# Kernel tuning notes

Hardware: AMD Instinct MI355X
Metric: run time of the kernel (lower is better)

Reference implementation:

```python
import jax, jax.numpy as jnp
import numpy as np

H = 16          # n_heads
D_MODEL = 1024
DK = D_MODEL // H  # 64
N = 2048        # total tokens (module flattens batch*seq)
NEG = -1000000000.0


def setup_inputs() -> dict:
    key = jax.random.key(0)
    ks = jax.random.split(key, 12)
    s = 1.0 / np.sqrt(D_MODEL)
    inp = {
        "query": jax.random.normal(ks[0], (N, D_MODEL), jnp.float32),
        "key": jax.random.normal(ks[1], (N, D_MODEL), jnp.float32),
        "value": jax.random.normal(ks[2], (N, D_MODEL), jnp.float32),
        "mask": jax.random.randint(ks[3], (1, N), 0, 2, jnp.int32),
        "Wq": jax.random.normal(ks[4], (D_MODEL, D_MODEL), jnp.float32) * s,
        "bq": jax.random.normal(ks[5], (D_MODEL,), jnp.float32) * 0.01,
        "Wk": jax.random.normal(ks[6], (D_MODEL, D_MODEL), jnp.float32) * s,
        "bk": jax.random.normal(ks[7], (D_MODEL,), jnp.float32) * 0.01,
        "Wv": jax.random.normal(ks[8], (D_MODEL, D_MODEL), jnp.float32) * s,
        "bv": jax.random.normal(ks[9], (D_MODEL,), jnp.float32) * 0.01,
        "Wo": jax.random.normal(ks[10], (D_MODEL, D_MODEL), jnp.float32) * s,
        "bo": jax.random.normal(ks[11], (D_MODEL,), jnp.float32) * 0.01,
    }
    return inp


def reference(query, key, value, mask, Wq, bq, Wk, bk, Wv, bv, Wo, bo):
    # Linear projections (torch Linear: x @ W.T + b), then split heads: (N, d_model) -> (h, N, d_k)
    def split_heads(x):
        return x.reshape(-1, H, DK).transpose(1, 0, 2)

    q = split_heads(query @ Wq.T + bq)
    k = split_heads(key @ Wk.T + bk)
    v = split_heads(value @ Wv.T + bv)

    # scaled dot-product attention: scores (h, N, N)
    scores = jnp.einsum("hnd,hmd->hnm", q, k) / jnp.sqrt(jnp.asarray(DK, q.dtype))
    # mask: (1, N) --unsqueeze(1)--> (1, 1, N), broadcast over (h, N, N)
    scores = jnp.where(mask[None, :, :] == 0, jnp.asarray(NEG, scores.dtype), scores)
    p_attn = jax.nn.softmax(scores, axis=-1)  # dropout identity (eval mode)

    x = jnp.einsum("hnm,hmd->hnd", p_attn, v)  # (h, N, d_k)
    x = x.transpose(1, 0, 2).reshape(-1, H * DK)  # (N, d_model)
    out = x @ Wo.T + bo
    return (out, p_attn)
```

## Files before the change

kernel.cpp:

```cpp
#include <hip/hip_runtime.h>


#define NTOK 2048
#define DMODEL 1024
#define NHEAD 16
#define DKH 64

typedef __attribute__((ext_vector_type(8))) short bf16x8;
typedef __attribute__((ext_vector_type(4))) float f32x4;

__device__ __forceinline__ unsigned short f2bf(float x) {
  unsigned int u = __builtin_bit_cast(unsigned int, x);
  u += 0x7fffu + ((u >> 16) & 1u);
  return (unsigned short)(u >> 16);
}

struct GemmP {
  const void* A[3];
  const void* B[3];
  const float* bias[3];
  long long sA, sB, sC;
  int lda, ldb, ldc;
  int M, Nn, K;
  const int* mask;
  float scale;
  void* C;
};

template<int ROWS, bool F32>
__device__ __forceinline__ void stage_tile(char* lds, const char* gsrc, int ld, int k0, int tid) {
  if constexpr (F32) {
    const float* src = (const float*)gsrc;
#pragma unroll
    for (int c = 0; c < ROWS / 16; ++c) {
      int cid = c * 256 + tid;
      int row = cid >> 4;
      int ck = cid & 15;
      float4 v = *(const float4*)(src + (size_t)row * ld + k0 + ck * 4);
      ushort4 h;
      h.x = f2bf(v.x); h.y = f2bf(v.y); h.z = f2bf(v.z); h.w = f2bf(v.w);
      int off = row * 128 + ((ck * 8) ^ ((row & 7) << 4));
      *(ushort4*)(lds + off) = h;
    }
  } else {
    const unsigned short* src = (const unsigned short*)gsrc;
#pragma unroll
    for (int c = 0; c < ROWS / 32; ++c) {
      int cid = c * 256 + tid;
      int row = cid >> 3;
      int ck = cid & 7;
      uint4 v = *(const uint4*)(src + (size_t)row * ld + k0 + ck * 8);
      int off = row * 128 + ((ck * 16) ^ ((row & 7) << 4));
      *(uint4*)(lds + off) = v;
    }
  }
}

__device__ __forceinline__ void stage_v256(char* lds, const unsigned short* src, int ld, int tid) {
#pragma unroll
  for (int c = 0; c < 4; ++c) {
    int cid = c * 256 + tid;
    int row = cid >> 4;
    int ck = cid & 15;
    uint4 v = *(const uint4*)(src + (size_t)row * ld + ck * 8);
    int off = row * 256 + ((ck * 16) ^ ((row & 7) << 4));
    *(uint4*)(lds + off) = v;
  }
}

__device__ __forceinline__ bf16x8 ldsfrag(const char* lds, int r, int kb) {
  return *(const bf16x8*)(lds + r * 128 + (kb ^ ((r & 7) << 4)));
}
__device__ __forceinline__ bf16x8 ldsfrag256(const char* lds, int r, int kb) {
  return *(const bf16x8*)(lds + r * 256 + (kb ^ ((r & 7) << 4)));
}

template<int BM, int BN, bool AF32, bool BF32, bool OUTF32, bool MASKED>
__global__ __launch_bounds__(256) void gemm_bt(GemmP P) {
  constexpr int BK = 64;
  constexpr int WM = BM / 2, WN = BN / 2, FM = WM / 16, FN = WN / 16;
  __shared__ char ldsA[BM * 128];
  __shared__ char ldsB[BN * 128];
  const int tid = threadIdx.x;
  const int z = blockIdx.z;
  const bool sel3 = (gridDim.z == 3);
  const int zi = sel3 ? z : 0;
  const int ntn = P.Nn / BN;
  const int bm = (int)blockIdx.x / ntn;
  const int bn = (int)blockIdx.x % ntn;
  const int m0 = bm * BM, n0 = bn * BN;

  const long long zA = sel3 ? 0 : (long long)z * P.sA;
  const long long zB = sel3 ? 0 : (long long)z * P.sB;
  const char* Ab = (const char*)P.A[zi] + ((long long)m0 * P.lda + zA) * (AF32 ? 4 : 2);
  const char* Bb = (const char*)P.B[zi] + ((long long)n0 * P.ldb + zB) * (BF32 ? 4 : 2);

  f32x4 acc[FM][FN] = {};
  const int lane = tid & 63;
  const int wm = (tid >> 6) >> 1, wn = (tid >> 6) & 1;

  for (int k0 = 0; k0 < P.K; k0 += BK) {
    stage_tile<BM, AF32>(ldsA, Ab, P.lda, k0, tid);
    stage_tile<BN, BF32>(ldsB, Bb, P.ldb, k0, tid);
    __syncthreads();
#pragma unroll
    for (int kk = 0; kk < 2; ++kk) {
      const int kb = kk * 64 + ((lane >> 4) * 16);
      bf16x8 a[FM], b[FN];
#pragma unroll
      for (int i = 0; i < FM; ++i) a[i] = ldsfrag(ldsA, wm * WM + i * 16 + (lane & 15), kb);
#pragma unroll
      for (int j = 0; j < FN; ++j) b[j] = ldsfrag(ldsB, wn * WN + j * 16 + (lane & 15), kb);
#pragma unroll
      for (int i = 0; i < FM; ++i)
#pragma unroll
        for (int j = 0; j < FN; ++j)
          acc[i][j] = __builtin_amdgcn_mfma_f32_16x16x32_bf16(a[i], b[j], acc[i][j], 0, 0, 0);
    }
    __syncthreads();
  }

  char* Cb = (char*)P.C + ((long long)z * P.sC) * (OUTF32 ? 4 : 2);
  const int rbase = m0 + wm * WM + ((lane >> 4) << 2);
  const int cbase = n0 + wn * WN + (lane & 15);
#pragma unroll
  for (int j = 0; j < FN; ++j) {
    const int col = cbase + j * 16;
    const float badd = P.bias[zi] ? P.bias[zi][col] : 0.0f;
    const bool msk = MASKED ? (P.mask[col] == 0) : false;
#pragma unroll
    for (int i = 0; i < FM; ++i) {
#pragma unroll
      for (int rg = 0; rg < 4; ++rg) {
        const int row = rbase + i * 16 + rg;
        float v = acc[i][j][rg] * P.scale + badd;
        if (MASKED && msk) v = -1000000000.0f;
        if constexpr (OUTF32)
          ((float*)Cb)[(size_t)row * P.ldc + col] = v;
        else
          ((unsigned short*)Cb)[(size_t)row * P.ldc + col] = f2bf(v);
      }
    }
  }
}

__global__ __launch_bounds__(256) void transpose_v(const unsigned short* __restrict__ VP,
                                                   unsigned short* __restrict__ VT) {
  __shared__ unsigned short t[64][72];
  const int h = blockIdx.y;
  const int n0 = blockIdx.x * 64;
  const int tid = threadIdx.x;
  const int rr = tid >> 3;
  const int cc = (tid & 7) * 8;
#pragma unroll
  for (int ps = 0; ps < 2; ++ps) {
    const int r = ps * 32 + rr;
    const unsigned short* src = VP + (size_t)(n0 + r) * DMODEL + h * DKH + cc;
    ushort4 a = *(const ushort4*)src;
    ushort4 b = *(const ushort4*)(src + 4);
    t[cc + 0][r] = a.x; t[cc + 1][r] = a.y; t[cc + 2][r] = a.z; t[cc + 3][r] = a.w;
    t[cc + 4][r] = b.x; t[cc + 5][r] = b.y; t[cc + 6][r] = b.z; t[cc + 7][r] = b.w;
  }
  __syncthreads();
#pragma unroll
  for (int ps = 0; ps < 2; ++ps) {
    const int d = ps * 32 + rr;
    unsigned short* dst = VT + ((size_t)h * DKH + d) * NTOK + n0 + cc;
    ushort4 a, b;
    a.x = t[d][cc + 0]; a.y = t[d][cc + 1]; a.z = t[d][cc + 2]; a.w = t[d][cc + 3];
    b.x = t[d][cc + 4]; b.y = t[d][cc + 5]; b.z = t[d][cc + 6]; b.w = t[d][cc + 7];
    *(ushort4*)dst = a;
    *(ushort4*)(dst + 4) = b;
  }
}

__global__ __launch_bounds__(256) void attn_fused(const unsigned short* __restrict__ QP,
                                                  const unsigned short* __restrict__ KP,
                                                  const unsigned short* __restrict__ VT,
                                                  const int* __restrict__ mask,
                                                  float* __restrict__ p,
                                                  unsigned short* __restrict__ XB) {
  __shared__ char ldsQ[64 * 128];
  __shared__ char ldsK[128 * 128];
  __shared__ char ldsV[64 * 256];
  __shared__ char ldsP[64 * 256];
  const int tid = threadIdx.x;
  const int lane = tid & 63;
  const int w = tid >> 6;
  const int l15 = lane & 15, lhi = lane >> 4;
  const int h = blockIdx.y;
  const int q0 = blockIdx.x * 64;
  const int mrow = w * 16 + l15;

  stage_tile<64, false>(ldsQ, (const char*)(QP + (size_t)q0 * DMODEL + h * DKH), DMODEL, 0, tid);
  __syncthreads();
  bf16x8 qf[2];
  qf[0] = ldsfrag(ldsQ, mrow, lhi * 16);
  qf[1] = ldsfrag(ldsQ, mrow, 64 + lhi * 16);

  float rsum = 0.0f;
  for (int it = 0; it < 16; ++it) {
    const int j0 = it * 128;
    __syncthreads();
    stage_tile<128, false>(ldsK, (const char*)(KP + (size_t)j0 * DMODEL + h * DKH), DMODEL, 0, tid);
    __syncthreads();
    f32x4 sacc[8] = {};
#pragma unroll
    for (int kk = 0; kk < 2; ++kk) {
#pragma unroll
      for (int js = 0; js < 8; ++js) {
        bf16x8 kf = ldsfrag(ldsK, js * 16 + l15, kk * 64 + lhi * 16);
        sacc[js] = __builtin_amdgcn_mfma_f32_16x16x32_bf16(kf, qf[kk], sacc[js], 0, 0, 0);
      }
    }
#pragma unroll
    for (int js = 0; js < 8; ++js) {
      int4 mv = *(const int4*)(mask + j0 + js * 16 + lhi * 4);
      rsum += (mv.x ? __expf(sacc[js][0] * 0.125f) : 0.0f);
      rsum += (mv.y ? __expf(sacc[js][1] * 0.125f) : 0.0f);
      rsum += (mv.z ? __expf(sacc[js][2] * 0.125f) : 0.0f);
      rsum += (mv.w ? __expf(sacc[js][3] * 0.125f) : 0.0f);
    }
  }
  rsum += __shfl_xor(rsum, 16, 64);
  rsum += __shfl_xor(rsum, 32, 64);
  const float rinv = 1.0f / rsum;

  float* prow = p + ((size_t)h * NTOK + q0 + mrow) * NTOK;
  f32x4 xacc[4] = {};
  for (int it = 0; it < 16; ++it) {
    const int j0 = it * 128;
    __syncthreads();
    stage_tile<128, false>(ldsK, (const char*)(KP + (size_t)j0 * DMODEL + h * DKH), DMODEL, 0, tid);
    stage_v256(ldsV, VT + (size_t)h * DKH * NTOK + j0, NTOK, tid);
    __syncthreads();
    f32x4 sacc[8] = {};
#pragma unroll
    for (int kk = 0; kk < 2; ++kk) {
#pragma unroll
      for (int js = 0; js < 8; ++js) {
        bf16x8 kf = ldsfrag(ldsK, js * 16 + l15, kk * 64 + lhi * 16);
        sacc[js] = __builtin_amdgcn_mfma_f32_16x16x32_bf16(kf, qf[kk], sacc[js], 0, 0, 0);
      }
    }
#pragma unroll
    for (int js = 0; js < 8; ++js) {
      int4 mv = *(const int4*)(mask + j0 + js * 16 + lhi * 4);
      float4 e;
      e.x = mv.x ? __expf(sacc[js][0] * 0.125f) * rinv : 0.0f;
      e.y = mv.y ? __expf(sacc[js][1] * 0.125f) * rinv : 0.0f;
      e.z = mv.z ? __expf(sacc[js][2] * 0.125f) * rinv : 0.0f;
      e.w = mv.w ? __expf(sacc[js][3] * 0.125f) * rinv : 0.0f;
      *(float4*)(prow + j0 + js * 16 + lhi * 4) = e;
      ushort4 pb;
      pb.x = f2bf(e.x); pb.y = f2bf(e.y); pb.z = f2bf(e.z); pb.w = f2bf(e.w);
      const int jl = (js * 16 + lhi * 4) * 2;
      *(ushort4*)(ldsP + mrow * 256 + (jl ^ ((mrow & 7) << 4))) = pb;
    }
    __syncthreads();
#pragma unroll
    for (int jk = 0; jk < 4; ++jk) {
      bf16x8 pf = ldsfrag256(ldsP, mrow, jk * 64 + lhi * 16);
#pragma unroll
      for (int dd = 0; dd < 4; ++dd) {
        bf16x8 vf = ldsfrag256(ldsV, dd * 16 + l15, jk * 64 + lhi * 16);
        xacc[dd] = __builtin_amdgcn_mfma_f32_16x16x32_bf16(vf, pf, xacc[dd], 0, 0, 0);
      }
    }
  }

  unsigned short* xrow = XB + (size_t)(q0 + mrow) * DMODEL + h * DKH;
#pragma unroll
  for (int dd = 0; dd < 4; ++dd) {
    ushort4 xb;
    xb.x = f2bf(xacc[dd][0]); xb.y = f2bf(xacc[dd][1]);
    xb.z = f2bf(xacc[dd][2]); xb.w = f2bf(xacc[dd][3]);
    *(ushort4*)(xrow + dd * 16 + lhi * 4) = xb;
  }
}

extern "C" void kernel_launch(void* const* d_in, const int* in_sizes, int n_in,
                              void* d_out, int out_size, void* d_ws, size_t ws_size,
                              hipStream_t stream) {
  (void)in_sizes; (void)n_in; (void)out_size; (void)ws_size;
  const float* query = (const float*)d_in[0];
  const float* key_  = (const float*)d_in[1];
  const float* value = (const float*)d_in[2];
  const int*   mask  = (const int*)d_in[3];
  const float* Wq = (const float*)d_in[4];
  const float* bq = (const float*)d_in[5];
  const float* Wk = (const float*)d_in[6];
  const float* bk = (const float*)d_in[7];
  const float* Wv = (const float*)d_in[8];
  const float* bv = (const float*)d_in[9];
  const float* Wo = (const float*)d_in[10];
  const float* bo = (const float*)d_in[11];

  float* out = (float*)d_out;
  float* p = out + (size_t)NTOK * DMODEL;

  char* ws = (char*)d_ws;
  unsigned short* QP = (unsigned short*)(ws);
  unsigned short* KP = (unsigned short*)(ws + (4u << 20));
  unsigned short* VP = (unsigned short*)(ws + (8u << 20));
  unsigned short* VT = (unsigned short*)(ws + (12u << 20));
  unsigned short* XB = (unsigned short*)(ws + (16u << 20));

  {
    GemmP P = {};
    P.A[0] = query; P.A[1] = key_; P.A[2] = value;
    P.B[0] = Wq; P.B[1] = Wk; P.B[2] = Wv;
    P.bias[0] = bq; P.bias[1] = bk; P.bias[2] = bv;
    P.sA = 0; P.sB = 0; P.sC = (long long)NTOK * DMODEL;
    P.lda = DMODEL; P.ldb = DMODEL; P.ldc = DMODEL;
    P.M = NTOK; P.Nn = DMODEL; P.K = DMODEL;
    P.mask = nullptr; P.scale = 1.0f; P.C = QP;
    gemm_bt<64, 128, true, true, false, false>
        <<<dim3((NTOK / 64) * (DMODEL / 128), 1, 3), 256, 0, stream>>>(P);
  }
  transpose_v<<<dim3(NTOK / 64, NHEAD), 256, 0, stream>>>(VP, VT);
  attn_fused<<<dim3(NTOK / 64, NHEAD), 256, 0, stream>>>(QP, KP, VT, mask, p, XB);
  {
    GemmP P = {};
    P.A[0] = XB; P.B[0] = Wo; P.bias[0] = bo;
    P.sA = 0; P.sB = 0; P.sC = 0;
    P.lda = DMODEL; P.ldb = DMODEL; P.ldc = DMODEL;
    P.M = NTOK; P.Nn = DMODEL; P.K = DMODEL;
    P.mask = nullptr; P.scale = 1.0f; P.C = out;
    gemm_bt<64, 128, false, true, true, false>
        <<<dim3((NTOK / 64) * (DMODEL / 128), 1, 1), 256, 0, stream>>>(P);
  }
}
```

Baseline: 170.9 us.

## Pre-convert inputs to bf16, use async global-to-LDS loads and double-buffered attention

Adds a single conversion kernel that turns activations and weights into bf16 and builds an additive mask bias. The GEMMs now stage tiles with global_load_lds asynchronous copies, and the QKV GEMM uses larger M tiles and writes V already transposed, so the separate transpose kernel is gone. The attention kernel uses 64-key tiles with double-buffered K/V in LDS, exp2 with a folded scale and log-sum, and nontemporal stores for the probability matrix. The trade-off is an extra conversion pass over all inputs and weights plus more workspace memory.

```diff
diff --git a/kernel.cpp b/kernel.cpp
--- a/kernel.cpp
+++ b/kernel.cpp
@@ -15,102 +15,97 @@
   return (unsigned short)(u >> 16);
 }
 
-struct GemmP {
-  const void* A[3];
-  const void* B[3];
-  const float* bias[3];
-  long long sA, sB, sC;
-  int lda, ldb, ldc;
-  int M, Nn, K;
-  const int* mask;
-  float scale;
-  void* C;
-};
-
-template<int ROWS, bool F32>
-__device__ __forceinline__ void stage_tile(char* lds, const char* gsrc, int ld, int k0, int tid) {
-  if constexpr (F32) {
-    const float* src = (const float*)gsrc;
-#pragma unroll
-    for (int c = 0; c < ROWS / 16; ++c) {
-      int cid = c * 256 + tid;
-      int row = cid >> 4;
-      int ck = cid & 15;
-      float4 v = *(const float4*)(src + (size_t)row * ld + k0 + ck * 4);
-      ushort4 h;
-      h.x = f2bf(v.x); h.y = f2bf(v.y); h.z = f2bf(v.z); h.w = f2bf(v.w);
-      int off = row * 128 + ((ck * 8) ^ ((row & 7) << 4));
-      *(ushort4*)(lds + off) = h;
-    }
-  } else {
-    const unsigned short* src = (const unsigned short*)gsrc;
-#pragma unroll
-    for (int c = 0; c < ROWS / 32; ++c) {
-      int cid = c * 256 + tid;
-      int row = cid >> 3;
-      int ck = cid & 7;
-      uint4 v = *(const uint4*)(src + (size_t)row * ld + k0 + ck * 8);
-      int off = row * 128 + ((ck * 16) ^ ((row & 7) << 4));
-      *(uint4*)(lds + off) = v;
-    }
-  }
-}
-
-__device__ __forceinline__ void stage_v256(char* lds, const unsigned short* src, int ld, int tid) {
-#pragma unroll
-  for (int c = 0; c < 4; ++c) {
-    int cid = c * 256 + tid;
-    int row = cid >> 4;
-    int ck = cid & 15;
-    uint4 v = *(const uint4*)(src + (size_t)row * ld + ck * 8);
-    int off = row * 256 + ((ck * 16) ^ ((row & 7) << 4));
-    *(uint4*)(lds + off) = v;
+__device__ __forceinline__ void gl16(const void* g, void* l) {
+  __builtin_amdgcn_global_load_lds((const __attribute__((address_space(1))) void*)g,
+                                   (__attribute__((address_space(3))) void*)l, 16, 0, 0);
+}
+
+template<int ROWS>
+__device__ __forceinline__ void stage_async(const unsigned short* src, int ld,
+                                            char* lds, int w, int lane) {
+  constexpr int RPW = ROWS / 4;
+#pragma unroll
+  for (int i = 0; i < RPW / 8; ++i) {
+    const int row = w * RPW + i * 8 + (lane >> 3);
+    const unsigned short* g = src + (size_t)row * ld + (((lane & 7) ^ (row & 7)) * 8);
+    gl16(g, lds + (size_t)(w * RPW + i * 8) * 128);
   }
 }
 
 __device__ __forceinline__ bf16x8 ldsfrag(const char* lds, int r, int kb) {
   return *(const bf16x8*)(lds + r * 128 + (kb ^ ((r & 7) << 4)));
 }
-__device__ __forceinline__ bf16x8 ldsfrag256(const char* lds, int r, int kb) {
-  return *(const bf16x8*)(lds + r * 256 + (kb ^ ((r & 7) << 4)));
-}
-
-template<int BM, int BN, bool AF32, bool BF32, bool OUTF32, bool MASKED>
-__global__ __launch_bounds__(256) void gemm_bt(GemmP P) {
-  constexpr int BK = 64;
-  constexpr int WM = BM / 2, WN = BN / 2, FM = WM / 16, FN = WN / 16;
+
+struct CvtP {
+  const float* src[7];
+  unsigned short* dst[7];
+  int n8[8];
+  const int* mask;
+  float* mbias;
+};
+__global__ __launch_bounds__(256) void cvt_all(CvtP P) {
+  const int a = blockIdx.z;
+  const int i = blockIdx.x * 256 + threadIdx.x;
+  if (i >= P.n8[a]) return;
+  if (a == 7) {
+#pragma unroll
+    for (int r = 0; r < 8; ++r) {
+      int j = i * 8 + r;
+      P.mbias[j] = P.mask[j] ? 0.0f : -1e30f;
+    }
+    return;
+  }
+  const float4* s = (const float4*)P.src[a];
+  float4 v0 = s[i * 2], v1 = s[i * 2 + 1];
+  ushort4 h0, h1;
+  h0.x = f2bf(v0.x); h0.y = f2bf(v0.y); h0.z = f2bf(v0.z); h0.w = f2bf(v0.w);
+  h1.x = f2bf(v1.x); h1.y = f2bf(v1.y); h1.z = f2bf(v1.z); h1.w = f2bf(v1.w);
+  ((ushort4*)P.dst[a])[i * 2] = h0;
+  ((ushort4*)P.dst[a])[i * 2 + 1] = h1;
+}
+
+struct GemmP2 {
+  const unsigned short* A[3];
+  const unsigned short* B[3];
+  const float* bias[3];
+  unsigned short* Cb16;
+  float* Cf32;
+  unsigned short* VTd;
+  long long sC;
+  int lda, ldb, ldc, Nn, K;
+};
+
+template<int BM, bool OUTF32, bool VTRANS>
+__global__ __launch_bounds__(256) void gemm_glds(GemmP2 P) {
+  constexpr int BN = 128, WN = 64, FN = 4;
+  constexpr int WM = BM / 2, FM = WM / 16;
   __shared__ char ldsA[BM * 128];
   __shared__ char ldsB[BN * 128];
   const int tid = threadIdx.x;
+  const int lane = tid & 63, w = tid >> 6;
+  const int l15 = lane & 15, lhi = lane >> 4;
   const int z = blockIdx.z;
-  const bool sel3 = (gridDim.z == 3);
-  const int zi = sel3 ? z : 0;
+  const int zi = (gridDim.z == 3) ? z : 0;
   const int ntn = P.Nn / BN;
-  const int bm = (int)blockIdx.x / ntn;
-  const int bn = (int)blockIdx.x % ntn;
-  const int m0 = bm * BM, n0 = bn * BN;
-
-  const long long zA = sel3 ? 0 : (long long)z * P.sA;
-  const long long zB = sel3 ? 0 : (long long)z * P.sB;
-  const char* Ab = (const char*)P.A[zi] + ((long long)m0 * P.lda + zA) * (AF32 ? 4 : 2);
-  const char* Bb = (const char*)P.B[zi] + ((long long)n0 * P.ldb + zB) * (BF32 ? 4 : 2);
+  const int m0 = ((int)blockIdx.x / ntn) * BM;
+  const int n0 = ((int)blockIdx.x % ntn) * BN;
+  const unsigned short* Ab = P.A[zi] + (size_t)m0 * P.lda;
+  const unsigned short* Bb = P.B[zi] + (size_t)n0 * P.ldb;
+  const int wm = w >> 1, wn = w & 1;
 
   f32x4 acc[FM][FN] = {};
-  const int lane = tid & 63;
-  const int wm = (tid >> 6) >> 1, wn = (tid >> 6) & 1;
-
-  for (int k0 = 0; k0 < P.K; k0 += BK) {
-    stage_tile<BM, AF32>(ldsA, Ab, P.lda, k0, tid);
-    stage_tile<BN, BF32>(ldsB, Bb, P.ldb, k0, tid);
+  for (int k0 = 0; k0 < P.K; k0 += 64) {
+    stage_async<BM>(Ab + k0, P.lda, ldsA, w, lane);
+    stage_async<BN>(Bb + k0, P.ldb, ldsB, w, lane);
     __syncthreads();
 #pragma unroll
     for (int kk = 0; kk < 2; ++kk) {
-      const int kb = kk * 64 + ((lane >> 4) * 16);
+      const int kb = kk * 64 + lhi * 16;
       bf16x8 a[FM], b[FN];
 #pragma unroll
-      for (int i = 0; i < FM; ++i) a[i] = ldsfrag(ldsA, wm * WM + i * 16 + (lane & 15), kb);
-#pragma unroll
-      for (int j = 0; j < FN; ++j) b[j] = ldsfrag(ldsB, wn * WN + j * 16 + (lane & 15), kb);
+      for (int i = 0; i < FM; ++i) a[i] = ldsfrag(ldsA, wm * WM + i * 16 + l15, kb);
+#pragma unroll
+      for (int j = 0; j < FN; ++j) b[j] = ldsfrag(ldsB, wn * WN + j * 16 + l15, kb);
 #pragma unroll
       for (int i = 0; i < FM; ++i)
 #pragma unroll
@@ -120,153 +115,144 @@
     __syncthreads();
   }
 
-  char* Cb = (char*)P.C + ((long long)z * P.sC) * (OUTF32 ? 4 : 2);
-  const int rbase = m0 + wm * WM + ((lane >> 4) << 2);
-  const int cbase = n0 + wn * WN + (lane & 15);
+  const int rbase = m0 + wm * WM + lhi * 4;
+  const int cbase = n0 + wn * WN + l15;
+  if (VTRANS && z == 2) {
+#pragma unroll
+    for (int j = 0; j < FN; ++j) {
+      const int col = cbase + j * 16;
+      const float badd = P.bias[zi][col];
+#pragma unroll
+      for (int i = 0; i < FM; ++i) {
+        ushort4 t;
+        t.x = f2bf(acc[i][j][0] + badd); t.y = f2bf(acc[i][j][1] + badd);
+        t.z = f2bf(acc[i][j][2] + badd); t.w = f2bf(acc[i][j][3] + badd);
+        *(ushort4*)(P.VTd + (size_t)col * NTOK + rbase + i * 16) = t;
+      }
+    }
+    return;
+  }
 #pragma unroll
   for (int j = 0; j < FN; ++j) {
     const int col = cbase + j * 16;
     const float badd = P.bias[zi] ? P.bias[zi][col] : 0.0f;
-    const bool msk = MASKED ? (P.mask[col] == 0) : false;
 #pragma unroll
     for (int i = 0; i < FM; ++i) {
 #pragma unroll
       for (int rg = 0; rg < 4; ++rg) {
         const int row = rbase + i * 16 + rg;
-        float v = acc[i][j][rg] * P.scale + badd;
-        if (MASKED && msk) v = -1000000000.0f;
+        const float v = acc[i][j][rg] + badd;
         if constexpr (OUTF32)
-          ((float*)Cb)[(size_t)row * P.ldc + col] = v;
+          P.Cf32[(size_t)row * P.ldc + col] = v;
         else
-          ((unsigned short*)Cb)[(size_t)row * P.ldc + col] = f2bf(v);
-      }
-    }
-  }
-}
-
-__global__ __launch_bounds__(256) void transpose_v(const unsigned short* __restrict__ VP,
-                                                   unsigned short* __restrict__ VT) {
-  __shared__ unsigned short t[64][72];
-  const int h = blockIdx.y;
-  const int n0 = blockIdx.x * 64;
+          P.Cb16[(size_t)z * P.sC + (size_t)row * P.ldc + col] = f2bf(v);
+      }
+    }
+  }
+}
+
+__global__ __launch_bounds__(256) void attn2(const unsigned short* __restrict__ QP,
+                                             const unsigned short* __restrict__ KP,
+                                             const unsigned short* __restrict__ VT,
+                                             const float* __restrict__ mbias,
+                                             float* __restrict__ p,
+                                             unsigned short* __restrict__ XB) {
+  __shared__ char ldsK[2][64 * 128];
+  __shared__ char ldsV[2][64 * 128];
+  __shared__ char ldsP[64 * 128];
   const int tid = threadIdx.x;
-  const int rr = tid >> 3;
-  const int cc = (tid & 7) * 8;
-#pragma unroll
-  for (int ps = 0; ps < 2; ++ps) {
-    const int r = ps * 32 + rr;
-    const unsigned short* src = VP + (size_t)(n0 + r) * DMODEL + h * DKH + cc;
-    ushort4 a = *(const ushort4*)src;
-    ushort4 b = *(const ushort4*)(src + 4);
-    t[cc + 0][r] = a.x; t[cc + 1][r] = a.y; t[cc + 2][r] = a.z; t[cc + 3][r] = a.w;
-    t[cc + 4][r] = b.x; t[cc + 5][r] = b.y; t[cc + 6][r] = b.z; t[cc + 7][r] = b.w;
-  }
-  __syncthreads();
-#pragma unroll
-  for (int ps = 0; ps < 2; ++ps) {
-    const int d = ps * 32 + rr;
-    unsigned short* dst = VT + ((size_t)h * DKH + d) * NTOK + n0 + cc;
-    ushort4 a, b;
-    a.x = t[d][cc + 0]; a.y = t[d][cc + 1]; a.z = t[d][cc + 2]; a.w = t[d][cc + 3];
-    b.x = t[d][cc + 4]; b.y = t[d][cc + 5]; b.z = t[d][cc + 6]; b.w = t[d][cc + 7];
-    *(ushort4*)dst = a;
-    *(ushort4*)(dst + 4) = b;
-  }
-}
-
-__global__ __launch_bounds__(256) void attn_fused(const unsigned short* __restrict__ QP,
-                                                  const unsigned short* __restrict__ KP,
-                                                  const unsigned short* __restrict__ VT,
-                                                  const int* __restrict__ mask,
-                                                  float* __restrict__ p,
-                                                  unsigned short* __restrict__ XB) {
-  __shared__ char ldsQ[64 * 128];
-  __shared__ char ldsK[128 * 128];
-  __shared__ char ldsV[64 * 256];
-  __shared__ char ldsP[64 * 256];
-  const int tid = threadIdx.x;
-  const int lane = tid & 63;
-  const int w = tid >> 6;
+  const int lane = tid & 63, w = tid >> 6;
   const int l15 = lane & 15, lhi = lane >> 4;
   const int h = blockIdx.y;
   const int q0 = blockIdx.x * 64;
   const int mrow = w * 16 + l15;
-
-  stage_tile<64, false>(ldsQ, (const char*)(QP + (size_t)q0 * DMODEL + h * DKH), DMODEL, 0, tid);
+  constexpr float CEXP = 0.1803368801111204f;
+
+  stage_async<64>(QP + (size_t)q0 * DMODEL + h * DKH, DMODEL, ldsP, w, lane);
   __syncthreads();
   bf16x8 qf[2];
-  qf[0] = ldsfrag(ldsQ, mrow, lhi * 16);
-  qf[1] = ldsfrag(ldsQ, mrow, 64 + lhi * 16);
+  qf[0] = ldsfrag(ldsP, mrow, lhi * 16);
+  qf[1] = ldsfrag(ldsP, mrow, 64 + lhi * 16);
+  __syncthreads();
+
+  const unsigned short* Kh = KP + h * DKH;
+  const unsigned short* Vh = VT + (size_t)h * DKH * NTOK;
 
   float rsum = 0.0f;
-  for (int it = 0; it < 16; ++it) {
-    const int j0 = it * 128;
+  stage_async<64>(Kh, DMODEL, ldsK[0], w, lane);
+  __syncthreads();
+  int b = 0;
+  for (int it = 0; it < 32; ++it) {
+    if (it < 31)
+      stage_async<64>(Kh + (size_t)(it + 1) * 64 * DMODEL, DMODEL, ldsK[b ^ 1], w, lane);
+    f32x4 sacc[4] = {};
+#pragma unroll
+    for (int kk = 0; kk < 2; ++kk)
+#pragma unroll
+      for (int js = 0; js < 4; ++js) {
+        bf16x8 kf = ldsfrag(ldsK[b], js * 16 + l15, kk * 64 + lhi * 16);
+        sacc[js] = __builtin_amdgcn_mfma_f32_16x16x32_bf16(kf, qf[kk], sacc[js], 0, 0, 0);
+      }
+    const float* mb = mbias + it * 64;
+#pragma unroll
+    for (int js = 0; js < 4; ++js) {
+      float4 m4 = *(const float4*)(mb + js * 16 + lhi * 4);
+      rsum += exp2f(sacc[js][0] * CEXP + m4.x);
+      rsum += exp2f(sacc[js][1] * CEXP + m4.y);
+      rsum += exp2f(sacc[js][2] * CEXP + m4.z);
+      rsum += exp2f(sacc[js][3] * CEXP + m4.w);
+    }
     __syncthreads();
-    stage_tile<128, false>(ldsK, (const char*)(KP + (size_t)j0 * DMODEL + h * DKH), DMODEL, 0, tid);
-    __syncthreads();
-    f32x4 sacc[8] = {};
-#pragma unroll
-    for (int kk = 0; kk < 2; ++kk) {
-#pragma unroll
-      for (int js = 0; js < 8; ++js) {
-        bf16x8 kf = ldsfrag(ldsK, js * 16 + l15, kk * 64 + lhi * 16);
-        sacc[js] = __builtin_amdgcn_mfma_f32_16x16x32_bf16(kf, qf[kk], sacc[js], 0, 0, 0);
-      }
-    }
-#pragma unroll
-    for (int js = 0; js < 8; ++js) {
-      int4 mv = *(const int4*)(mask + j0 + js * 16 + lhi * 4);
-      rsum += (mv.x ? __expf(sacc[js][0] * 0.125f) : 0.0f);
-      rsum += (mv.y ? __expf(sacc[js][1] * 0.125f) : 0.0f);
-      rsum += (mv.z ? __expf(sacc[js][2] * 0.125f) : 0.0f);
-      rsum += (mv.w ? __expf(sacc[js][3] * 0.125f) : 0.0f);
-    }
+    b ^= 1;
   }
   rsum += __shfl_xor(rsum, 16, 64);
   rsum += __shfl_xor(rsum, 32, 64);
-  const float rinv = 1.0f / rsum;
+  const float lr = -log2f(rsum);
 
   float* prow = p + ((size_t)h * NTOK + q0 + mrow) * NTOK;
   f32x4 xacc[4] = {};
-  for (int it = 0; it < 16; ++it) {
-    const int j0 = it * 128;
+  stage_async<64>(Kh, DMODEL, ldsK[0], w, lane);
+  stage_async<64>(Vh, NTOK, ldsV[0], w, lane);
+  __syncthreads();
+  b = 0;
+  for (int it = 0; it < 32; ++it) {
+    if (it < 31) {
+      stage_async<64>(Kh + (size_t)(it + 1) * 64 * DMODEL, DMODEL, ldsK[b ^ 1], w, lane);
+      stage_async<64>(Vh + (it + 1) * 64, NTOK, ldsV[b ^ 1], w, lane);
+    }
+    f32x4 sacc[4] = {};
+#pragma unroll
+    for (int kk = 0; kk < 2; ++kk)
+#pragma unroll
+      for (int js = 0; js < 4; ++js) {
+        bf16x8 kf = ldsfrag(ldsK[b], js * 16 + l15, kk * 64 + lhi * 16);
+        sacc[js] = __builtin_amdgcn_mfma_f32_16x16x32_bf16(kf, qf[kk], sacc[js], 0, 0, 0);
+      }
+    const float* mb = mbias + it * 64;
+#pragma unroll
+    for (int js = 0; js < 4; ++js) {
+      float4 m4 = *(const float4*)(mb + js * 16 + lhi * 4);
+      f32x4 e;
+      e[0] = exp2f(sacc[js][0] * CEXP + (m4.x + lr));
+      e[1] = exp2f(sacc[js][1] * CEXP + (m4.y + lr));
+      e[2] = exp2f(sacc[js][2] * CEXP + (m4.z + lr));
+      e[3] = exp2f(sacc[js][3] * CEXP + (m4.w + lr));
+      __builtin_nontemporal_store(e, (f32x4*)(prow + it * 64 + js * 16 + lhi * 4));
+      ushort4 pb;
+      pb.x = f2bf(e[0]); pb.y = f2bf(e[1]); pb.z = f2bf(e[2]); pb.w = f2bf(e[3]);
+      *(ushort4*)(ldsP + mrow * 128 + ((js * 32 + lhi * 8) ^ ((mrow & 7) << 4))) = pb;
+    }
+#pragma unroll
+    for (int jk = 0; jk < 2; ++jk) {
+      bf16x8 pf = ldsfrag(ldsP, mrow, jk * 64 + lhi * 16);
+#pragma unroll
+      for (int dd = 0; dd < 4; ++dd) {
+        bf16x8 vf = ldsfrag(ldsV[b], dd * 16 + l15, jk * 64 + lhi * 16);
+        xacc[dd] = __builtin_amdgcn_mfma_f32_16x16x32_bf16(vf, pf, xacc[dd], 0, 0, 0);
+      }
+    }
     __syncthreads();
-    stage_tile<128, false>(ldsK, (const char*)(KP + (size_t)j0 * DMODEL + h * DKH), DMODEL, 0, tid);
-    stage_v256(ldsV, VT + (size_t)h * DKH * NTOK + j0, NTOK, tid);
-    __syncthreads();
-    f32x4 sacc[8] = {};
-#pragma unroll
-    for (int kk = 0; kk < 2; ++kk) {
-#pragma unroll
-      for (int js = 0; js < 8; ++js) {
-        bf16x8 kf = ldsfrag(ldsK, js * 16 + l15, kk * 64 + lhi * 16);
-        sacc[js] = __builtin_amdgcn_mfma_f32_16x16x32_bf16(kf, qf[kk], sacc[js], 0, 0, 0);
-      }
-    }
-#pragma unroll
-    for (int js = 0; js < 8; ++js) {
-      int4 mv = *(const int4*)(mask + j0 + js * 16 + lhi * 4);
-      float4 e;
-      e.x = mv.x ? __expf(sacc[js][0] * 0.125f) * rinv : 0.0f;
-      e.y = mv.y ? __expf(sacc[js][1] * 0.125f) * rinv : 0.0f;
-      e.z = mv.z ? __expf(sacc[js][2] * 0.125f) * rinv : 0.0f;
-      e.w = mv.w ? __expf(sacc[js][3] * 0.125f) * rinv : 0.0f;
-      *(float4*)(prow + j0 + js * 16 + lhi * 4) = e;
-      ushort4 pb;
-      pb.x = f2bf(e.x); pb.y = f2bf(e.y); pb.z = f2bf(e.z); pb.w = f2bf(e.w);
-      const int jl = (js * 16 + lhi * 4) * 2;
-      *(ushort4*)(ldsP + mrow * 256 + (jl ^ ((mrow & 7) << 4))) = pb;
-    }
-    __syncthreads();
-#pragma unroll
-    for (int jk = 0; jk < 4; ++jk) {
-      bf16x8 pf = ldsfrag256(ldsP, mrow, jk * 64 + lhi * 16);
-#pragma unroll
-      for (int dd = 0; dd < 4; ++dd) {
-        bf16x8 vf = ldsfrag256(ldsV, dd * 16 + l15, jk * 64 + lhi * 16);
-        xacc[dd] = __builtin_amdgcn_mfma_f32_16x16x32_bf16(vf, pf, xacc[dd], 0, 0, 0);
-      }
-    }
+    b ^= 1;
   }
 
   unsigned short* xrow = XB + (size_t)(q0 + mrow) * DMODEL + h * DKH;
@@ -300,34 +286,49 @@
   float* p = out + (size_t)NTOK * DMODEL;
 
   char* ws = (char*)d_ws;
-  unsigned short* QP = (unsigned short*)(ws);
-  unsigned short* KP = (unsigned short*)(ws + (4u << 20));
-  unsigned short* VP = (unsigned short*)(ws + (8u << 20));
-  unsigned short* VT = (unsigned short*)(ws + (12u << 20));
-  unsigned short* XB = (unsigned short*)(ws + (16u << 20));
+  unsigned short* QP  = (unsigned short*)(ws);
+  unsigned short* KP  = (unsigned short*)(ws + (4u << 20));
+  unsigned short* VT  = (unsigned short*)(ws + (8u << 20));
+  unsigned short* XB  = (unsigned short*)(ws + (12u << 20));
+  unsigned short* qB  = (unsigned short*)(ws + (16u << 20));
+  unsigned short* kB  = (unsigned short*)(ws + (20u << 20));
+  unsigned short* vB  = (unsigned short*)(ws + (24u << 20));
+  unsigned short* WqB = (unsigned short*)(ws + (28u << 20));
+  unsigned short* WkB = (unsigned short*)(ws + (30u << 20));
+  unsigned short* WvB = (unsigned short*)(ws + (32u << 20));
+  unsigned short* WoB = (unsigned short*)(ws + (34u << 20));
+  float* mbias = (float*)(ws + (36u << 20));
 
   {
-    GemmP P = {};
-    P.A[0] = query; P.A[1] = key_; P.A[2] = value;
-    P.B[0] = Wq; P.B[1] = Wk; P.B[2] = Wv;
+    CvtP C = {};
+    C.src[0] = query; C.dst[0] = qB;  C.n8[0] = NTOK * DMODEL / 8;
+    C.src[1] = key_;  C.dst[1] = kB;  C.n8[1] = NTOK * DMODEL / 8;
+    C.src[2] = value; C.dst[2] = vB;  C.n8[2] = NTOK * DMODEL / 8;
+    C.src[3] = Wq;    C.dst[3] = WqB; C.n8[3] = DMODEL * DMODEL / 8;
+    C.src[4] = Wk;    C.dst[4] = WkB; C.n8[4] = DMODEL * DMODEL / 8;
+    C.src[5] = Wv;    C.dst[5] = WvB; C.n8[5] = DMODEL * DMODEL / 8;
+    C.src[6] = Wo;    C.dst[6] = WoB; C.n8[6] = DMODEL * DMODEL / 8;
+    C.n8[7] = NTOK / 8;
+    C.mask = mask; C.mbias = mbias;
+    cvt_all<<<dim3(1024, 1, 8), 256, 0, stream>>>(C);
+  }
+  {
+    GemmP2 P = {};
+    P.A[0] = qB; P.A[1] = kB; P.A[2] = vB;
+    P.B[0] = WqB; P.B[1] = WkB; P.B[2] = WvB;
     P.bias[0] = bq; P.bias[1] = bk; P.bias[2] = bv;
-    P.sA = 0; P.sB = 0; P.sC = (long long)NTOK * DMODEL;
-    P.lda = DMODEL; P.ldb = DMODEL; P.ldc = DMODEL;
-    P.M = NTOK; P.Nn = DMODEL; P.K = DMODEL;
-    P.mask = nullptr; P.scale = 1.0f; P.C = QP;
-    gemm_bt<64, 128, true, true, false, false>
-        <<<dim3((NTOK / 64) * (DMODEL / 128), 1, 3), 256, 0, stream>>>(P);
-  }
-  transpose_v<<<dim3(NTOK / 64, NHEAD), 256, 0, stream>>>(VP, VT);
-  attn_fused<<<dim3(NTOK / 64, NHEAD), 256, 0, stream>>>(QP, KP, VT, mask, p, XB);
+    P.Cb16 = QP; P.VTd = VT; P.sC = (long long)NTOK * DMODEL;
+    P.lda = DMODEL; P.ldb = DMODEL; P.ldc = DMODEL; P.Nn = DMODEL; P.K = DMODEL;
+    gemm_glds<128, false, true>
+        <<<dim3((NTOK / 128) * (DMODEL / 128), 1, 3), 256, 0, stream>>>(P);
+  }
+  attn2<<<dim3(NTOK / 64, NHEAD), 256, 0, stream>>>(QP, KP, VT, mbias, p, XB);
   {
-    GemmP P = {};
-    P.A[0] = XB; P.B[0] = Wo; P.bias[0] = bo;
-    P.sA = 0; P.sB = 0; P.sC = 0;
-    P.lda = DMODEL; P.ldb = DMODEL; P.ldc = DMODEL;
-    P.M = NTOK; P.Nn = DMODEL; P.K = DMODEL;
-    P.mask = nullptr; P.scale = 1.0f; P.C = out;
-    gemm_bt<64, 128, false, true, true, false>
+    GemmP2 P = {};
+    P.A[0] = XB; P.B[0] = WoB; P.bias[0] = bo;
+    P.Cf32 = out; P.sC = 0;
+    P.lda = DMODEL; P.ldb = DMODEL; P.ldc = DMODEL; P.Nn = DMODEL; P.K = DMODEL;
+    gemm_glds<64, true, false>
         <<<dim3((NTOK / 64) * (DMODEL / 128), 1, 1), 256, 0, stream>>>(P);
   }
 }
```

After: 196.0 us (median of 3 runs). +14.7%, slower.
